# Kernel optimization log

Measured on AMD Instinct MI355X. Metric: run time of the kernel, lower is better.

## Reference

```python
import jax, jax.numpy as jnp
import numpy as np

N = 100000      # nodes
E = 3200000     # edges (avg degree 32)
F_IN = 128      # num_node_features
H = 128         # hidden_channels


def gcn_conv(x, edge_index, W, b, n):
    """PyG-style GCNConv: linear transform, add self-loops, symmetric
    D^{-1/2} A D^{-1/2} normalization, scatter-add aggregation, bias."""
    h = x @ W  # [n, out]
    row, col = edge_index[0], edge_index[1]
    loop = jnp.arange(n, dtype=row.dtype)
    row = jnp.concatenate([row, loop])
    col = jnp.concatenate([col, loop])
    deg = jax.ops.segment_sum(jnp.ones(row.shape, h.dtype), col, num_segments=n)
    dinv = jnp.where(deg > 0, jax.lax.rsqrt(deg), 0.0)
    norm = dinv[row] * dinv[col]                 # [E+n]
    msg = h[row] * norm[:, None]                 # gather + scale
    out = jax.ops.segment_sum(msg, col, num_segments=n)  # scatter-add
    return out + b


def setup_inputs() -> dict:
    key = jax.random.key(0)
    ks = jax.random.split(key, 8)
    x = jax.random.normal(ks[0], (N, F_IN), jnp.float32)
    edge_index = jax.random.randint(ks[1], (2, E), 0, N, dtype=jnp.int32)
    s1 = 1.0 / np.sqrt(F_IN)
    s2 = 1.0 / np.sqrt(H)
    W1 = jax.random.normal(ks[2], (F_IN, H), jnp.float32) * s1
    b1 = jnp.zeros((H,), jnp.float32)
    W2 = jax.random.normal(ks[3], (H, H), jnp.float32) * s2
    b2 = jnp.zeros((H,), jnp.float32)
    Wl = jax.random.normal(ks[4], (H, 1), jnp.float32) * s2
    bl = jnp.zeros((1,), jnp.float32)
    return {"x": x, "edge_index": edge_index, "W1": W1, "b1": b1,
            "W2": W2, "b2": b2, "Wl": Wl, "bl": bl}


def reference(x, edge_index, W1, b1, W2, b2, Wl, bl):
    n = x.shape[0]
    h = jax.nn.relu(gcn_conv(x, edge_index, W1, b1, n))
    # dropout p=0.5 is identity in eval mode (training=False)
    h = jax.nn.relu(gcn_conv(h, edge_index, W2, b2, n))
    return jax.nn.sigmoid(h @ Wl + bl)  # [n, 1]
```

## Files before the change

### kernel.cpp

```cpp
#include <hip/hip_runtime.h>
#include <math.h>

#define FDIM 128
#define BKT_BITS 8
#define BKT_W (1 << BKT_BITS)
#define BIN_CHUNK 12544

typedef short bf16x8 __attribute__((ext_vector_type(8)));
typedef float f32x4 __attribute__((ext_vector_type(4)));
typedef float f32x2 __attribute__((ext_vector_type(2)));

union ABu { bf16x8 v; unsigned int u[4]; };
union F4u { float4 f; float a[4]; };

__device__ inline unsigned int pack_bf16x2(float a, float b) {
  unsigned int ua = __float_as_uint(a);
  unsigned int ub = __float_as_uint(b);
  ua = (ua + 0x7fffu + ((ua >> 16) & 1u)) >> 16;
  ub = (ub + 0x7fffu + ((ub >> 16) & 1u)) >> 16;
  return ua | (ub << 16);
}

__device__ inline unsigned char f32_to_fp8(float v) {
  return (unsigned char)(__builtin_amdgcn_cvt_pk_fp8_f32(v, v, 0, false) & 0xff);
}
__device__ inline float2 fp8x2_to_f32(unsigned int u) {
  f32x2 r = __builtin_amdgcn_cvt_pk_f32_fp8((int)u, false);
  return make_float2(r[0], r[1]);
}


__global__ __launch_bounds__(256)
void k_bhist(const int* __restrict__ col, int* __restrict__ gbcnt, int nE, int nb) {
  __shared__ int lds[512];
  for (int i = threadIdx.x; i < 512; i += 256) lds[i] = 0;
  __syncthreads();
  int stride = gridDim.x * blockDim.x;
  for (int e = blockIdx.x * blockDim.x + threadIdx.x; e < nE; e += stride)
    atomicAdd(&lds[col[e] >> BKT_BITS], 1);
  __syncthreads();
  for (int b = threadIdx.x; b < nb; b += 256) {
    int c = lds[b];
    if (c) atomicAdd(&gbcnt[b], c);
  }
}

__global__ __launch_bounds__(512)
void k_bscan(const int* __restrict__ gbcnt, int* __restrict__ gboff,
             int* __restrict__ gcur, int nb, int nE) {
  __shared__ int lds[512];
  int t = threadIdx.x;
  lds[t] = (t < nb) ? gbcnt[t] : 0;
  __syncthreads();
  for (int off = 1; off < 512; off <<= 1) {
    int x = (t >= off) ? lds[t - off] : 0;
    __syncthreads();
    lds[t] += x;
    __syncthreads();
  }
  if (t < nb) {
    int excl = (t == 0) ? 0 : lds[t - 1];
    gboff[t] = excl;
    gcur[t] = excl;
  }
  if (t == 0) gboff[nb] = nE;
}

__global__ __launch_bounds__(256)
void k_bin(const int* __restrict__ row, const int* __restrict__ col,
           int* __restrict__ gcur, int* __restrict__ pairs, int nE, int chunk, int nb) {
  __shared__ int bcnt[512];
  __shared__ int lcur[512];
  __shared__ int ecol[BIN_CHUNK];
  int e0 = blockIdx.x * chunk;
  int e1 = min(e0 + chunk, nE);
  int m = e1 - e0;
  for (int i = threadIdx.x; i < 512; i += 256) bcnt[i] = 0;
  for (int i = threadIdx.x; i < m; i += 256) ecol[i] = col[e0 + i];
  __syncthreads();
  for (int i = threadIdx.x; i < m; i += 256)
    atomicAdd(&bcnt[((unsigned)ecol[i]) >> BKT_BITS], 1);
  __syncthreads();
  for (int b = threadIdx.x; b < nb; b += 256) {
    int c = bcnt[b];
    lcur[b] = c ? atomicAdd(&gcur[b], c) : 0;
  }
  __syncthreads();
  for (int i = threadIdx.x; i < m; i += 256) {
    int c = ecol[i];
    int r = row[e0 + i];
    int p = atomicAdd(&lcur[((unsigned)c) >> BKT_BITS], 1);
    pairs[p] = r | ((c & (BKT_W - 1)) << 24);
  }
}

__global__ __launch_bounds__(256)
void k_fine(const int* __restrict__ pairs, const int* __restrict__ gboff,
            int* __restrict__ srcs, int* __restrict__ offs, int* __restrict__ cnt,
            float* __restrict__ dinv, int n) {
  __shared__ int lcnt[256];
  __shared__ int lcur[256];
  int b = blockIdx.x;
  int t = threadIdx.x;
  int ebase = gboff[b];
  int eend = gboff[b + 1];
  lcnt[t] = 0;
  __syncthreads();
  for (int e = ebase + t; e < eend; e += 256)
    atomicAdd(&lcnt[((unsigned)pairs[e]) >> 24], 1);
  __syncthreads();
  int orig = lcnt[t];
  for (int off = 1; off < 256; off <<= 1) {
    int x = (t >= off) ? lcnt[t - off] : 0;
    __syncthreads();
    lcnt[t] += x;
    __syncthreads();
  }
  int excl = lcnt[t] - orig;
  int v = (b << BKT_BITS) + t;
  if (v < n) {
    offs[v] = ebase + excl;
    cnt[v] = orig;
    dinv[v] = rsqrtf((float)(orig + 1));
  }
  lcur[t] = ebase + excl;
  __syncthreads();
  for (int e = ebase + t; e < eend; e += 256) {
    int pr = pairs[e];
    int p = atomicAdd(&lcur[((unsigned)pr) >> 24], 1);
    srcs[p] = pr & 0x00FFFFFF;
  }
}

#define STAGE_WT()                                                          \
  {                                                                         \
    int c = threadIdx.x & 127;                                              \
    for (int kp = (threadIdx.x >> 7); kp < 64; kp += 2) {                   \
      float w0 = W[(kp * 2) * 128 + c];                                     \
      float w1 = W[(kp * 2 + 1) * 128 + c];                                 \
      int unit = kp >> 2, dw = kp & 3;                                      \
      wlds[c * 64 + ((unit ^ (c & 15)) << 2) + dw] = pack_bf16x2(w0, w1);   \
    }                                                                       \
  }                                                                         \
  __syncthreads();

#define GEMM_BODY()                                                         \
  int l = threadIdx.x & 63;                                                 \
  int grp = l >> 4, c15 = l & 15;                                           \
  int rbase = blockIdx.x * 64 + (threadIdx.x >> 6) * 16;                    \
  F4u dv;                                                                   \
  dv.f = *(const float4*)(dinv + rbase + grp * 4);                          \
  f32x4 acc[8];                                                             \
  _Pragma("unroll")                                                         \
  for (int nt = 0; nt < 8; ++nt) acc[nt] = (f32x4){0.f, 0.f, 0.f, 0.f};    \
  _Pragma("unroll")                                                         \
  for (int nt = 0; nt < 8; ++nt) {                                          \
    _Pragma("unroll")                                                       \
    for (int ks = 0; ks < 4; ++ks) {                                        \
      ABu b;                                                                \
      b.v = *(const bf16x8*)&wlds[(nt * 16 + c15) * 64 +                    \
                                  ((((ks << 2) + grp) ^ c15) << 2)];        \
      acc[nt] = __builtin_amdgcn_mfma_f32_16x16x32_bf16(a[ks].v, b.v,       \
                                                        acc[nt], 0, 0, 0);  \
    }                                                                       \
  }                                                                         \
  _Pragma("unroll")                                                         \
  for (int nt = 0; nt < 8; ++nt) {                                          \
    _Pragma("unroll")                                                       \
    for (int i = 0; i < 4; ++i) {                                           \
      int r = rbase + grp * 4 + i;                                          \
      if (r < n) {                                                          \
        float v = acc[nt][i] * dv.a[i];                                     \
        out[(size_t)r * 128 + nt * 16 + c15] = f32_to_fp8(v);               \
      }                                                                     \
    }                                                                       \
  }

__global__ __launch_bounds__(256)
void k_gemm_mfma_f(const float* __restrict__ in, const float* __restrict__ W,
                   const float* __restrict__ dinv, unsigned char* __restrict__ out,
                   int n) {
  __shared__ unsigned int wlds[128 * 64];
  STAGE_WT();
  {
    int l0 = threadIdx.x & 63;
    int row = blockIdx.x * 64 + (threadIdx.x >> 6) * 16 + (l0 & 15);
    int rowc = min(row, n - 1);
    int grp0 = l0 >> 4;
    const float4* xr = (const float4*)(in + (size_t)rowc * 128);
    ABu a[4];
#pragma unroll
    for (int ks = 0; ks < 4; ++ks) {
      float4 f0 = xr[ks * 8 + grp0 * 2];
      float4 f1 = xr[ks * 8 + grp0 * 2 + 1];
      a[ks].u[0] = pack_bf16x2(f0.x, f0.y);
      a[ks].u[1] = pack_bf16x2(f0.z, f0.w);
      a[ks].u[2] = pack_bf16x2(f1.x, f1.y);
      a[ks].u[3] = pack_bf16x2(f1.z, f1.w);
    }
    GEMM_BODY();
  }
}

__global__ __launch_bounds__(256)
void k_gemm_mfma_b(const unsigned int* __restrict__ in, const float* __restrict__ W,
                   const float* __restrict__ dinv, unsigned char* __restrict__ out,
                   int n) {
  __shared__ unsigned int wlds[128 * 64];
  STAGE_WT();
  {
    int l0 = threadIdx.x & 63;
    int row = blockIdx.x * 64 + (threadIdx.x >> 6) * 16 + (l0 & 15);
    int rowc = min(row, n - 1);
    int grp0 = l0 >> 4;
    const unsigned int* hr = in + (size_t)rowc * 64;
    ABu a[4];
#pragma unroll
    for (int ks = 0; ks < 4; ++ks)
      a[ks].v = *(const bf16x8*)&hr[ks * 16 + grp0 * 4];
    GEMM_BODY();
  }
}

__device__ inline float2 agg_core(const unsigned short* __restrict__ sb,
                                  const int* __restrict__ offs,
                                  const int* __restrict__ cnt,
                                  const int* __restrict__ srcs,
                                  int v, int lane) {
  float2 acc;
  {
    float2 d = fp8x2_to_f32(sb[(size_t)v * 64 + lane]);
    acc = d;
  }
  int beg = offs[v];
  int m = cnt[v];
  for (int base = 0; base < m; base += 64) {
    int take = m - base;
    if (take > 64) take = 64;
    int idx = (lane < take) ? srcs[beg + base + lane] : 0;
    int it = 0;
    for (; it + 7 < take; it += 8) {
      int u0 = __shfl(idx, it, 64);
      int u1 = __shfl(idx, it + 1, 64);
      int u2 = __shfl(idx, it + 2, 64);
      int u3 = __shfl(idx, it + 3, 64);
      int u4 = __shfl(idx, it + 4, 64);
      int u5 = __shfl(idx, it + 5, 64);
      int u6 = __shfl(idx, it + 6, 64);
      int u7 = __shfl(idx, it + 7, 64);
      unsigned short p0 = sb[(size_t)u0 * 64 + lane];
      unsigned short p1 = sb[(size_t)u1 * 64 + lane];
      unsigned short p2 = sb[(size_t)u2 * 64 + lane];
      unsigned short p3 = sb[(size_t)u3 * 64 + lane];
      unsigned short p4 = sb[(size_t)u4 * 64 + lane];
      unsigned short p5 = sb[(size_t)u5 * 64 + lane];
      unsigned short p6 = sb[(size_t)u6 * 64 + lane];
      unsigned short p7 = sb[(size_t)u7 * 64 + lane];
      float2 d0 = fp8x2_to_f32(p0);
      float2 d1 = fp8x2_to_f32(p1);
      float2 d2 = fp8x2_to_f32(p2);
      float2 d3 = fp8x2_to_f32(p3);
      float2 d4 = fp8x2_to_f32(p4);
      float2 d5 = fp8x2_to_f32(p5);
      float2 d6 = fp8x2_to_f32(p6);
      float2 d7 = fp8x2_to_f32(p7);
      acc.x += ((d0.x + d1.x) + (d2.x + d3.x)) + ((d4.x + d5.x) + (d6.x + d7.x));
      acc.y += ((d0.y + d1.y) + (d2.y + d3.y)) + ((d4.y + d5.y) + (d6.y + d7.y));
    }
    for (; it < take; ++it) {
      int u = __shfl(idx, it, 64);
      float2 d = fp8x2_to_f32(sb[(size_t)u * 64 + lane]);
      acc.x += d.x;
      acc.y += d.y;
    }
  }
  return acc;
}

__global__ __launch_bounds__(256)
void k_agg_mid(const unsigned short* __restrict__ sb, const int* __restrict__ offs,
               const int* __restrict__ cnt, const int* __restrict__ srcs,
               const float* __restrict__ dinv, const float* __restrict__ bias,
               unsigned int* __restrict__ hb, int n) {
  int v = (int)(((size_t)blockIdx.x * blockDim.x + threadIdx.x) >> 6);
  if (v >= n) return;
  int lane = threadIdx.x & 63;
  float2 acc = agg_core(sb, offs, cnt, srcs, v, lane);
  float d = dinv[v];
  float2 b = ((const float2*)bias)[lane];
  float rx = fmaxf(acc.x * d + b.x, 0.0f);
  float ry = fmaxf(acc.y * d + b.y, 0.0f);
  hb[(size_t)v * 64 + lane] = pack_bf16x2(rx, ry);
}

__global__ __launch_bounds__(256)
void k_agg_head(const unsigned short* __restrict__ sb, const int* __restrict__ offs,
                const int* __restrict__ cnt, const int* __restrict__ srcs,
                const float* __restrict__ dinv, const float* __restrict__ bias,
                const float* __restrict__ Wl, const float* __restrict__ bl,
                float* __restrict__ out, int n) {
  int v = (int)(((size_t)blockIdx.x * blockDim.x + threadIdx.x) >> 6);
  if (v >= n) return;
  int lane = threadIdx.x & 63;
  float2 acc = agg_core(sb, offs, cnt, srcs, v, lane);
  float d = dinv[v];
  float2 b = ((const float2*)bias)[lane];
  float rx = fmaxf(acc.x * d + b.x, 0.0f);
  float ry = fmaxf(acc.y * d + b.y, 0.0f);
  float2 wv = ((const float2*)Wl)[lane];
  float p = rx * wv.x + ry * wv.y;
#pragma unroll
  for (int off = 32; off > 0; off >>= 1) p += __shfl_down(p, off, 64);
  if (lane == 0) {
    float z = p + bl[0];
    out[v] = 1.0f / (1.0f + expf(-z));
  }
}


extern "C" void kernel_launch(void* const* d_in, const int* in_sizes, int n_in,
                              void* d_out, int out_size, void* d_ws, size_t ws_size,
                              hipStream_t stream) {
  const float* x  = (const float*)d_in[0];
  const int*   ei = (const int*)d_in[1];
  const float* W1 = (const float*)d_in[2];
  const float* b1 = (const float*)d_in[3];
  const float* W2 = (const float*)d_in[4];
  const float* b2 = (const float*)d_in[5];
  const float* Wl = (const float*)d_in[6];
  const float* bl = (const float*)d_in[7];
  float* out = (float*)d_out;

  int n  = in_sizes[0] / FDIM;
  int nE = in_sizes[1] / 2;
  const int* row = ei;
  const int* col = ei + nE;
  int nb = (n + BKT_W - 1) >> BKT_BITS;

  unsigned char* s8 = (unsigned char*)d_ws;
  unsigned int* hb  = (unsigned int*)(s8 + (size_t)n * 128);
  float* dinv  = (float*)(hb + (size_t)n * 64);
  int*   cnt   = (int*)(dinv + n);
  int*   offs  = cnt + n;
  int*   srcs  = offs + n;
  int*   gbcnt = srcs + nE;
  int*   gboff = gbcnt + nb;
  int*   gcur  = gboff + nb + 1;
  int*   pairs = (int*)hb;

  hipMemsetAsync(gbcnt, 0, (size_t)nb * sizeof(int), stream);
  k_bhist<<<256, 256, 0, stream>>>(col, gbcnt, nE, nb);
  k_bscan<<<1, 512, 0, stream>>>(gbcnt, gboff, gcur, nb, nE);
  int chunk = (nE + 255) / 256;
  k_bin<<<256, 256, 0, stream>>>(row, col, gcur, pairs, nE, chunk, nb);
  k_fine<<<nb, 256, 0, stream>>>(pairs, gboff, srcs, offs, cnt, dinv, n);

  int gemm_grid = (n + 63) / 64;
  int wave_grid = (n + 3) / 4;
  k_gemm_mfma_f<<<gemm_grid, 256, 0, stream>>>(x, W1, dinv, s8, n);
  k_agg_mid<<<wave_grid, 256, 0, stream>>>((const unsigned short*)s8, offs, cnt, srcs, dinv, b1, hb, n);
  k_gemm_mfma_b<<<gemm_grid, 256, 0, stream>>>(hb, W2, dinv, s8, n);
  k_agg_head<<<wave_grid, 256, 0, stream>>>((const unsigned short*)s8, offs, cnt, srcs, dinv, b2, Wl, bl, out, n);
}
```

Measured before the change: 379.8 us.

## Split wave into half-waves gathering two neighbors with 4-byte fp8 loads

The aggregation kernels now have each half-wave (32 lanes) load a full 128-byte fp8 row using 4-byte loads per lane, so one wave gathers two neighbor rows per load instruction. A cross-half shuffle reduction at the end combines the partial sums. This is meant to cut gather instruction count and improve per-lane load width. The preprocessing kernels also get more parallelism: larger grids for histogram and binning, a halved bin chunk, and 1024-thread blocks in the fine sort.

```diff
diff --git a/kernel.cpp b/kernel.cpp
--- a/kernel.cpp
+++ b/kernel.cpp
@@ -4,7 +4,7 @@
 #define FDIM 128
 #define BKT_BITS 8
 #define BKT_W (1 << BKT_BITS)
-#define BIN_CHUNK 12544
+#define BIN_CHUNK 6272
 
 typedef short bf16x8 __attribute__((ext_vector_type(8)));
 typedef float f32x4 __attribute__((ext_vector_type(4)));
@@ -23,10 +23,6 @@
 
 __device__ inline unsigned char f32_to_fp8(float v) {
   return (unsigned char)(__builtin_amdgcn_cvt_pk_fp8_f32(v, v, 0, false) & 0xff);
-}
-__device__ inline float2 fp8x2_to_f32(unsigned int u) {
-  f32x2 r = __builtin_amdgcn_cvt_pk_f32_fp8((int)u, false);
-  return make_float2(r[0], r[1]);
 }
 
 
@@ -94,7 +90,7 @@
   }
 }
 
-__global__ __launch_bounds__(256)
+__global__ __launch_bounds__(1024)
 void k_fine(const int* __restrict__ pairs, const int* __restrict__ gboff,
             int* __restrict__ srcs, int* __restrict__ offs, int* __restrict__ cnt,
             float* __restrict__ dinv, int n) {
@@ -104,28 +100,30 @@
   int t = threadIdx.x;
   int ebase = gboff[b];
   int eend = gboff[b + 1];
-  lcnt[t] = 0;
-  __syncthreads();
-  for (int e = ebase + t; e < eend; e += 256)
+  if (t < 256) lcnt[t] = 0;
+  __syncthreads();
+  for (int e = ebase + t; e < eend; e += 1024)
     atomicAdd(&lcnt[((unsigned)pairs[e]) >> 24], 1);
   __syncthreads();
-  int orig = lcnt[t];
+  int orig = (t < 256) ? lcnt[t] : 0;
   for (int off = 1; off < 256; off <<= 1) {
-    int x = (t >= off) ? lcnt[t - off] : 0;
+    int x = (t < 256 && t >= off) ? lcnt[t - off] : 0;
     __syncthreads();
-    lcnt[t] += x;
+    if (t < 256) lcnt[t] += x;
     __syncthreads();
   }
-  int excl = lcnt[t] - orig;
-  int v = (b << BKT_BITS) + t;
-  if (v < n) {
-    offs[v] = ebase + excl;
-    cnt[v] = orig;
-    dinv[v] = rsqrtf((float)(orig + 1));
-  }
-  lcur[t] = ebase + excl;
-  __syncthreads();
-  for (int e = ebase + t; e < eend; e += 256) {
+  if (t < 256) {
+    int excl = lcnt[t] - orig;
+    int v = (b << BKT_BITS) + t;
+    if (v < n) {
+      offs[v] = ebase + excl;
+      cnt[v] = orig;
+      dinv[v] = rsqrtf((float)(orig + 1));
+    }
+    lcur[t] = ebase + excl;
+  }
+  __syncthreads();
+  for (int e = ebase + t; e < eend; e += 1024) {
     int pr = pairs[e];
     int p = atomicAdd(&lcur[((unsigned)pr) >> 24], 1);
     srcs[p] = pr & 0x00FFFFFF;
@@ -222,15 +220,19 @@
   }
 }
 
-__device__ inline float2 agg_core(const unsigned short* __restrict__ sb,
+__device__ inline float4 agg_core(const unsigned int* __restrict__ s4,
                                   const int* __restrict__ offs,
                                   const int* __restrict__ cnt,
                                   const int* __restrict__ srcs,
                                   int v, int lane) {
-  float2 acc;
-  {
-    float2 d = fp8x2_to_f32(sb[(size_t)v * 64 + lane]);
-    acc = d;
+  int cl = lane & 31;
+  int hf = lane >> 5;
+  float4 acc = make_float4(0.f, 0.f, 0.f, 0.f);
+  if (lane < 32) {
+    unsigned int q = s4[(size_t)v * 32 + cl];
+    f32x2 lo = __builtin_amdgcn_cvt_pk_f32_fp8((int)q, false);
+    f32x2 hi = __builtin_amdgcn_cvt_pk_f32_fp8((int)q, true);
+    acc = make_float4(lo[0], lo[1], hi[0], hi[1]);
   }
   int beg = offs[v];
   int m = cnt[v];
@@ -240,61 +242,77 @@
     int idx = (lane < take) ? srcs[beg + base + lane] : 0;
     int it = 0;
     for (; it + 7 < take; it += 8) {
-      int u0 = __shfl(idx, it, 64);
-      int u1 = __shfl(idx, it + 1, 64);
-      int u2 = __shfl(idx, it + 2, 64);
-      int u3 = __shfl(idx, it + 3, 64);
-      int u4 = __shfl(idx, it + 4, 64);
-      int u5 = __shfl(idx, it + 5, 64);
-      int u6 = __shfl(idx, it + 6, 64);
-      int u7 = __shfl(idx, it + 7, 64);
-      unsigned short p0 = sb[(size_t)u0 * 64 + lane];
-      unsigned short p1 = sb[(size_t)u1 * 64 + lane];
-      unsigned short p2 = sb[(size_t)u2 * 64 + lane];
-      unsigned short p3 = sb[(size_t)u3 * 64 + lane];
-      unsigned short p4 = sb[(size_t)u4 * 64 + lane];
-      unsigned short p5 = sb[(size_t)u5 * 64 + lane];
-      unsigned short p6 = sb[(size_t)u6 * 64 + lane];
-      unsigned short p7 = sb[(size_t)u7 * 64 + lane];
-      float2 d0 = fp8x2_to_f32(p0);
-      float2 d1 = fp8x2_to_f32(p1);
-      float2 d2 = fp8x2_to_f32(p2);
-      float2 d3 = fp8x2_to_f32(p3);
-      float2 d4 = fp8x2_to_f32(p4);
-      float2 d5 = fp8x2_to_f32(p5);
-      float2 d6 = fp8x2_to_f32(p6);
-      float2 d7 = fp8x2_to_f32(p7);
-      acc.x += ((d0.x + d1.x) + (d2.x + d3.x)) + ((d4.x + d5.x) + (d6.x + d7.x));
-      acc.y += ((d0.y + d1.y) + (d2.y + d3.y)) + ((d4.y + d5.y) + (d6.y + d7.y));
-    }
-    for (; it < take; ++it) {
+      int u0 = __shfl(idx, it + hf, 64);
+      int u1 = __shfl(idx, it + 2 + hf, 64);
+      int u2 = __shfl(idx, it + 4 + hf, 64);
+      int u3 = __shfl(idx, it + 6 + hf, 64);
+      unsigned int q0 = s4[(size_t)u0 * 32 + cl];
+      unsigned int q1 = s4[(size_t)u1 * 32 + cl];
+      unsigned int q2 = s4[(size_t)u2 * 32 + cl];
+      unsigned int q3 = s4[(size_t)u3 * 32 + cl];
+      f32x2 l0 = __builtin_amdgcn_cvt_pk_f32_fp8((int)q0, false);
+      f32x2 h0 = __builtin_amdgcn_cvt_pk_f32_fp8((int)q0, true);
+      f32x2 l1 = __builtin_amdgcn_cvt_pk_f32_fp8((int)q1, false);
+      f32x2 h1 = __builtin_amdgcn_cvt_pk_f32_fp8((int)q1, true);
+      f32x2 l2 = __builtin_amdgcn_cvt_pk_f32_fp8((int)q2, false);
+      f32x2 h2 = __builtin_amdgcn_cvt_pk_f32_fp8((int)q2, true);
+      f32x2 l3 = __builtin_amdgcn_cvt_pk_f32_fp8((int)q3, false);
+      f32x2 h3 = __builtin_amdgcn_cvt_pk_f32_fp8((int)q3, true);
+      acc.x += (l0[0] + l1[0]) + (l2[0] + l3[0]);
+      acc.y += (l0[1] + l1[1]) + (l2[1] + l3[1]);
+      acc.z += (h0[0] + h1[0]) + (h2[0] + h3[0]);
+      acc.w += (h0[1] + h1[1]) + (h2[1] + h3[1]);
+    }
+    for (; it + 1 < take; it += 2) {
+      int u = __shfl(idx, it + hf, 64);
+      unsigned int q = s4[(size_t)u * 32 + cl];
+      f32x2 lo = __builtin_amdgcn_cvt_pk_f32_fp8((int)q, false);
+      f32x2 hi = __builtin_amdgcn_cvt_pk_f32_fp8((int)q, true);
+      acc.x += lo[0]; acc.y += lo[1]; acc.z += hi[0]; acc.w += hi[1];
+    }
+    if (it < take) {
       int u = __shfl(idx, it, 64);
-      float2 d = fp8x2_to_f32(sb[(size_t)u * 64 + lane]);
-      acc.x += d.x;
-      acc.y += d.y;
-    }
-  }
+      if (lane < 32) {
+        unsigned int q = s4[(size_t)u * 32 + cl];
+        f32x2 lo = __builtin_amdgcn_cvt_pk_f32_fp8((int)q, false);
+        f32x2 hi = __builtin_amdgcn_cvt_pk_f32_fp8((int)q, true);
+        acc.x += lo[0]; acc.y += lo[1]; acc.z += hi[0]; acc.w += hi[1];
+      }
+    }
+  }
+  acc.x += __shfl_xor(acc.x, 32, 64);
+  acc.y += __shfl_xor(acc.y, 32, 64);
+  acc.z += __shfl_xor(acc.z, 32, 64);
+  acc.w += __shfl_xor(acc.w, 32, 64);
   return acc;
 }
 
 __global__ __launch_bounds__(256)
-void k_agg_mid(const unsigned short* __restrict__ sb, const int* __restrict__ offs,
+void k_agg_mid(const unsigned int* __restrict__ s4, const int* __restrict__ offs,
                const int* __restrict__ cnt, const int* __restrict__ srcs,
                const float* __restrict__ dinv, const float* __restrict__ bias,
                unsigned int* __restrict__ hb, int n) {
   int v = (int)(((size_t)blockIdx.x * blockDim.x + threadIdx.x) >> 6);
   if (v >= n) return;
   int lane = threadIdx.x & 63;
-  float2 acc = agg_core(sb, offs, cnt, srcs, v, lane);
-  float d = dinv[v];
-  float2 b = ((const float2*)bias)[lane];
-  float rx = fmaxf(acc.x * d + b.x, 0.0f);
-  float ry = fmaxf(acc.y * d + b.y, 0.0f);
-  hb[(size_t)v * 64 + lane] = pack_bf16x2(rx, ry);
-}
-
-__global__ __launch_bounds__(256)
-void k_agg_head(const unsigned short* __restrict__ sb, const int* __restrict__ offs,
+  float4 acc = agg_core(s4, offs, cnt, srcs, v, lane);
+  if (lane < 32) {
+    int cl = lane;
+    float d = dinv[v];
+    float4 bb = ((const float4*)bias)[cl];
+    float r0 = fmaxf(acc.x * d + bb.x, 0.0f);
+    float r1 = fmaxf(acc.y * d + bb.y, 0.0f);
+    float r2 = fmaxf(acc.z * d + bb.z, 0.0f);
+    float r3 = fmaxf(acc.w * d + bb.w, 0.0f);
+    uint2 pk;
+    pk.x = pack_bf16x2(r0, r1);
+    pk.y = pack_bf16x2(r2, r3);
+    ((uint2*)hb)[(size_t)v * 32 + cl] = pk;
+  }
+}
+
+__global__ __launch_bounds__(256)
+void k_agg_head(const unsigned int* __restrict__ s4, const int* __restrict__ offs,
                 const int* __restrict__ cnt, const int* __restrict__ srcs,
                 const float* __restrict__ dinv, const float* __restrict__ bias,
                 const float* __restrict__ Wl, const float* __restrict__ bl,
@@ -302,15 +320,24 @@
   int v = (int)(((size_t)blockIdx.x * blockDim.x + threadIdx.x) >> 6);
   if (v >= n) return;
   int lane = threadIdx.x & 63;
-  float2 acc = agg_core(sb, offs, cnt, srcs, v, lane);
-  float d = dinv[v];
-  float2 b = ((const float2*)bias)[lane];
-  float rx = fmaxf(acc.x * d + b.x, 0.0f);
-  float ry = fmaxf(acc.y * d + b.y, 0.0f);
-  float2 wv = ((const float2*)Wl)[lane];
-  float p = rx * wv.x + ry * wv.y;
-#pragma unroll
-  for (int off = 32; off > 0; off >>= 1) p += __shfl_down(p, off, 64);
+  float4 acc = agg_core(s4, offs, cnt, srcs, v, lane);
+  float p = 0.0f;
+  if (lane < 32) {
+    int cl = lane;
+    float d = dinv[v];
+    float4 bb = ((const float4*)bias)[cl];
+    float4 wv = ((const float4*)Wl)[cl];
+    float r0 = fmaxf(acc.x * d + bb.x, 0.0f);
+    float r1 = fmaxf(acc.y * d + bb.y, 0.0f);
+    float r2 = fmaxf(acc.z * d + bb.z, 0.0f);
+    float r3 = fmaxf(acc.w * d + bb.w, 0.0f);
+    p = r0 * wv.x + r1 * wv.y + r2 * wv.z + r3 * wv.w;
+  }
+  p += __shfl_down(p, 16, 64);
+  p += __shfl_down(p, 8, 64);
+  p += __shfl_down(p, 4, 64);
+  p += __shfl_down(p, 2, 64);
+  p += __shfl_down(p, 1, 64);
   if (lane == 0) {
     float z = p + bl[0];
     out[v] = 1.0f / (1.0f + expf(-z));
@@ -349,16 +376,16 @@
   int*   pairs = (int*)hb;
 
   hipMemsetAsync(gbcnt, 0, (size_t)nb * sizeof(int), stream);
-  k_bhist<<<256, 256, 0, stream>>>(col, gbcnt, nE, nb);
+  k_bhist<<<1024, 256, 0, stream>>>(col, gbcnt, nE, nb);
   k_bscan<<<1, 512, 0, stream>>>(gbcnt, gboff, gcur, nb, nE);
-  int chunk = (nE + 255) / 256;
-  k_bin<<<256, 256, 0, stream>>>(row, col, gcur, pairs, nE, chunk, nb);
-  k_fine<<<nb, 256, 0, stream>>>(pairs, gboff, srcs, offs, cnt, dinv, n);
+  int chunk = (nE + 511) / 512;
+  k_bin<<<512, 256, 0, stream>>>(row, col, gcur, pairs, nE, chunk, nb);
+  k_fine<<<nb, 1024, 0, stream>>>(pairs, gboff, srcs, offs, cnt, dinv, n);
 
   int gemm_grid = (n + 63) / 64;
   int wave_grid = (n + 3) / 4;
   k_gemm_mfma_f<<<gemm_grid, 256, 0, stream>>>(x, W1, dinv, s8, n);
-  k_agg_mid<<<wave_grid, 256, 0, stream>>>((const unsigned short*)s8, offs, cnt, srcs, dinv, b1, hb, n);
+  k_agg_mid<<<wave_grid, 256, 0, stream>>>((const unsigned int*)s8, offs, cnt, srcs, dinv, b1, hb, n);
   k_gemm_mfma_b<<<gemm_grid, 256, 0, stream>>>(hb, W2, dinv, s8, n);
-  k_agg_head<<<wave_grid, 256, 0, stream>>>((const unsigned short*)s8, offs, cnt, srcs, dinv, b2, Wl, bl, out, n);
-}
+  k_agg_head<<<wave_grid, 256, 0, stream>>>((const unsigned int*)s8, offs, cnt, srcs, dinv, b2, Wl, bl, out, n);
+}
```

New measurement: 375.1 us. About the same (-1.3%).
